# Kernel optimization log

Measured on AMD Instinct MI355X. Metric: run time of the kernel, lower is better.

The kernel has to match this reference:

```python
import jax, jax.numpy as jnp
import numpy as np

B = 262144
L = 12      # seq_len
P = 4       # num_ports
H = 64      # hidden_dim
S = 3       # num_stages
EPS = 1e-8


def setup_inputs() -> dict:
    key = jax.random.key(0)
    ks = jax.random.split(key, 8)
    def w(k, shape, fan_in):
        return jax.random.normal(k, shape, dtype=jnp.float32) / np.sqrt(fan_in)
    return {
        "y_real": jax.random.normal(ks[0], (B, L), dtype=jnp.float32),
        "y_imag": jax.random.normal(ks[1], (B, L), dtype=jnp.float32),
        # weights batched over (stage, port, real/imag branch)
        "W1": w(ks[2], (S, P, 2, 2 * L, H), 2 * L),
        "b1": w(ks[3], (S, P, 2, H), 2 * L),
        "W2": w(ks[4], (S, P, 2, H, H), H),
        "b2": w(ks[5], (S, P, 2, H), H),
        "W3": w(ks[6], (S, P, 2, H, L), H),
        "b3": w(ks[7], (S, P, 2, L), H),
    }


def reference(y_real, y_imag, W1, b1, W2, b2, W3, b3):
    # energy normalization: e = sqrt(mean(|y|^2))
    e = jnp.sqrt(jnp.mean(y_real * y_real + y_imag * y_imag, axis=-1, keepdims=True))  # (B,1)
    yr = y_real / (e + EPS)
    yi = y_imag / (e + EPS)

    n_stages, n_ports = W1.shape[0], W1.shape[1]
    fr = jnp.broadcast_to(yr[:, None, :], (yr.shape[0], n_ports, yr.shape[1]))  # (B,P,L)
    fi = jnp.broadcast_to(yi[:, None, :], (yi.shape[0], n_ports, yi.shape[1]))

    for s in range(n_stages):
        x = jnp.concatenate([fr, fi], axis=-1)                       # (B,P,2L) = cat(real, imag)
        h = jax.nn.relu(jnp.einsum('bpi,pcih->bpch', x, W1[s]) + b1[s])   # (B,P,2,H)
        h = jax.nn.relu(jnp.einsum('bpch,pchg->bpcg', h, W2[s]) + b2[s])  # (B,P,2,H)
        out = jnp.einsum('bpch,pchl->bpcl', h, W3[s]) + b3[s]        # (B,P,2,L)
        fr, fi = out[:, :, 0, :], out[:, :, 1, :]
        # residual coupling: residual = y_norm - sum_p features_p
        rr = yr - fr.sum(axis=1)
        ri = yi - fi.sum(axis=1)
        fr = fr + rr[:, None, :]
        fi = fi + ri[:, None, :]

    fr = fr * e[:, None, :]
    fi = fi * e[:, None, :]
    # complex output represented as trailing real/imag channel: (B,P,L,2)
    return jnp.stack([fr, fi], axis=-1)
```

## Files before the change

kernel.cpp:

```cpp
#include <hip/hip_runtime.h>
#include <hip/hip_bf16.h>

typedef __attribute__((ext_vector_type(8))) short bf16x8;
typedef __attribute__((ext_vector_type(4))) float f32x4;
typedef __attribute__((ext_vector_type(4))) unsigned int u32x4;
typedef unsigned long long ull;

#define RT 64
#define NB (262144 / RT)
#define XSTR 32
#define NFRAG 19

#define X_OFF 0
#define O_OFF 16384
#define Y_OFF 41344
#define E_OFF 47488
#define SMEM_BYTES 47744

__device__ __forceinline__ unsigned pk2(float lo, float hi) {
  union { float f; unsigned u; } a, b;
  a.f = lo; b.f = hi;
  return __builtin_amdgcn_perm(b.u + 0x8000u, a.u + 0x8000u, 0x07060302u);
}
__device__ __forceinline__ unsigned pk2t(float lo, float hi) {
  union { float f; unsigned u; } a, b;
  a.f = lo; b.f = hi;
  return __builtin_amdgcn_perm(b.u, a.u, 0x07060302u);
}
__device__ __forceinline__ bf16x8 mkfrag(unsigned w0, unsigned w1, unsigned w2, unsigned w3) {
  union { bf16x8 v; unsigned u[4]; } U;
  U.u[0] = w0; U.u[1] = w1; U.u[2] = w2; U.u[3] = w3;
  return U.v;
}
__device__ __forceinline__ f32x4 mfma16(bf16x8 a, bf16x8 b, f32x4 c) {
  return __builtin_amdgcn_mfma_f32_16x16x32_bf16(a, b, c, 0, 0, 0);
}

__global__ void wpack(const float* __restrict__ W1, const float* __restrict__ b1,
                      const float* __restrict__ W2, const float* __restrict__ b2,
                      const float* __restrict__ W3, const float* __restrict__ b3,
                      u32x4* __restrict__ ws)
{
  const int pc = blockIdx.x;
  const int lane = threadIdx.x;
  const int q = lane & 15, g = lane >> 4;
  int mpsi[4];
  #pragma unroll
  for (int mt = 0; mt < 4; ++mt)
    mpsi[mt] = 32*(mt>>1) + 8*(q>>2) + 4*(mt&1) + (q&3);

  const float* W1g = W1 + pc * 24 * 64;
  const float* b1g = b1 + pc * 64;
  const float* W2g = W2 + pc * 64 * 64;
  const float* b2g = b2 + pc * 64;
  const float* W3g = W3 + pc * 64 * 12;
  const float* b3g = b3 + pc * 12;
  u32x4* dst = ws + pc * NFRAG * 64 + lane;

  #pragma unroll
  for (int mt = 0; mt < 4; ++mt) {
    unsigned u[4];
    #pragma unroll
    for (int wq = 0; wq < 4; ++wq) {
      int k0 = 8*g + 2*wq;
      float v0 = (k0 < 24) ? W1g[k0*64 + mpsi[mt]] : ((k0 == 24) ? b1g[mpsi[mt]] : 0.f);
      float v1 = (k0+1 < 24) ? W1g[(k0+1)*64 + mpsi[mt]] : 0.f;
      u[wq] = pk2(v0, v1);
    }
    u32x4 t; t[0]=u[0]; t[1]=u[1]; t[2]=u[2]; t[3]=u[3];
    dst[mt * 64] = t;
  }
  #pragma unroll
  for (int kt = 0; kt < 2; ++kt)
    #pragma unroll
    for (int mt = 0; mt < 4; ++mt) {
      unsigned u[4];
      #pragma unroll
      for (int wq = 0; wq < 4; ++wq) {
        int k0 = 32*kt + 8*g + 2*wq;
        u[wq] = pk2(W2g[k0*64 + mpsi[mt]], W2g[(k0+1)*64 + mpsi[mt]]);
      }
      u32x4 t; t[0]=u[0]; t[1]=u[1]; t[2]=u[2]; t[3]=u[3];
      dst[(4 + kt*4 + mt) * 64] = t;
    }
  #pragma unroll
  for (int kt = 0; kt < 2; ++kt) {
    unsigned u[4];
    #pragma unroll
    for (int wq = 0; wq < 4; ++wq) {
      int k0 = 32*kt + 8*g + 2*wq;
      float v0 = (q < 12) ? W3g[k0*12 + q]     : 0.f;
      float v1 = (q < 12) ? W3g[(k0+1)*12 + q] : 0.f;
      u[wq] = pk2(v0, v1);
    }
    u32x4 t; t[0]=u[0]; t[1]=u[1]; t[2]=u[2]; t[3]=u[3];
    dst[(12 + kt) * 64] = t;
  }
  #pragma unroll
  for (int mt = 0; mt < 4; ++mt) {
    f32x4 bv;
    #pragma unroll
    for (int r = 0; r < 4; ++r) bv[r] = b2g[32*(mt>>1) + 8*g + 4*(mt&1) + r];
    union { f32x4 f; u32x4 u; } U; U.f = bv;
    dst[(14 + mt) * 64] = U.u;
  }
  {
    f32x4 bv;
    #pragma unroll
    for (int r = 0; r < 4; ++r) {
      int m = 4*g + r;
      bv[r] = (m < 12) ? b3g[m] : 0.f;
    }
    union { f32x4 f; u32x4 u; } U; U.f = bv;
    dst[18 * 64] = U.u;
  }
}

__global__ __launch_bounds__(256, 3) void rrsep(
    const float* __restrict__ y_real, const float* __restrict__ y_imag,
    const u32x4* __restrict__ wsf, float* __restrict__ out)
{
  __shared__ __align__(16) char smem[SMEM_BYTES];
  unsigned short* xs = (unsigned short*)(smem + X_OFF);
  float*          os = (float*)(smem + O_OFF);
  float*          ysf = (float*)(smem + Y_OFF);
  float*          es = (float*)(smem + E_OFF);

  const int tid  = (int)threadIdx.x;
  const int lane = tid & 63;
  const int p    = tid >> 6;
  const int q    = lane & 15;
  const int g    = lane >> 4;
  const long r0  = (long)blockIdx.x * RT;

  {
    float* stg = (float*)smem;
    if (tid < 192) {
      ((f32x4*)stg)[tid]         = ((const f32x4*)(y_real + r0 * 12))[tid];
      ((f32x4*)(stg + 768))[tid] = ((const f32x4*)(y_imag + r0 * 12))[tid];
    }
    __syncthreads();
    float yv[24]; float ev = 0.f, inv = 0.f;
    if (tid < RT) {
      float acc = 0.f;
      #pragma unroll
      for (int l = 0; l < 12; ++l) {
        yv[l]      = stg[tid * 12 + l];
        yv[12 + l] = stg[768 + tid * 12 + l];
        acc += yv[l] * yv[l] + yv[12 + l] * yv[12 + l];
      }
      ev  = sqrtf(acc * (1.f / 12.f));
      inv = 1.f / (ev + 1e-8f);
    }
    __syncthreads();
    if (tid < RT) {
      es[tid] = ev;
      #pragma unroll
      for (int i = 0; i < 6; ++i) {
        f32x4 t;
        t[0] = yv[4*i+0] * inv; t[1] = yv[4*i+1] * inv;
        t[2] = yv[4*i+2] * inv; t[3] = yv[4*i+3] * inv;
        int l0 = 4*i;
        float* yr = ysf + ((l0 < 12) ? (0 * RT + tid) * 12 + l0 : (1 * RT + tid) * 12 + (l0 - 12));
        *(f32x4*)yr = t;
      }
      unsigned pkw[12];
      #pragma unroll
      for (int j = 0; j < 12; ++j) pkw[j] = pk2(yv[2*j] * inv, yv[2*j+1] * inv);
      #pragma unroll
      for (int p2 = 0; p2 < 4; ++p2) {
        u32x4* xr = (u32x4*)(xs + (p2 * RT + tid) * XSTR);
        u32x4 t0; t0[0]=pkw[0]; t0[1]=pkw[1]; t0[2]=pkw[2]; t0[3]=pkw[3];
        u32x4 t1; t1[0]=pkw[4]; t1[1]=pkw[5]; t1[2]=pkw[6]; t1[3]=pkw[7];
        u32x4 t2; t2[0]=pkw[8]; t2[1]=pkw[9]; t2[2]=pkw[10]; t2[3]=pkw[11];
        u32x4 t3; t3[0]=pk2(1.f, 0.f); t3[1]=0u; t3[2]=0u; t3[3]=0u;
        xr[0]=t0; xr[1]=t1; xr[2]=t2; xr[3]=t3;
      }
    }
    __syncthreads();
  }

  #pragma unroll 1
  for (int s = 0; s < 3; ++s) {
    #pragma unroll 1
    for (int cc = 0; cc < 2; ++cc) {
      const int pc = (s * 4 + p) * 2 + cc;
      const u32x4* wb = wsf + pc * NFRAG * 64 + lane;

      bf16x8 w1f[4], w2f[2][4], w3f[2];
      f32x4 b2f[4], b3f;
      #pragma unroll
      for (int mt = 0; mt < 4; ++mt) {
        union { u32x4 u; bf16x8 v; } U; U.u = wb[mt * 64];
        w1f[mt] = U.v;
      }
      #pragma unroll
      for (int kt = 0; kt < 2; ++kt)
        #pragma unroll
        for (int mt = 0; mt < 4; ++mt) {
          union { u32x4 u; bf16x8 v; } U; U.u = wb[(4 + kt*4 + mt) * 64];
          w2f[kt][mt] = U.v;
        }
      #pragma unroll
      for (int kt = 0; kt < 2; ++kt) {
        union { u32x4 u; bf16x8 v; } U; U.u = wb[(12 + kt) * 64];
        w3f[kt] = U.v;
      }
      #pragma unroll
      for (int mt = 0; mt < 4; ++mt) {
        union { u32x4 u; f32x4 f; } U; U.u = wb[(14 + mt) * 64];
        b2f[mt] = U.f;
      }
      {
        union { u32x4 u; f32x4 f; } U; U.u = wb[18 * 64];
        b3f = U.f;
      }

      #pragma unroll 2
      for (int ch = 0; ch < RT / 16; ++ch) {
        const int row = ch * 16 + q;
        bf16x8 xb = *(const bf16x8*)(xs + (p * RT + row) * XSTR + 8 * g);

        f32x4 c1[4];
        #pragma unroll
        for (int mt = 0; mt < 4; ++mt) c1[mt] = mfma16(w1f[mt], xb, f32x4{0.f,0.f,0.f,0.f});

        bf16x8 fr1[2];
        #pragma unroll
        for (int kt = 0; kt < 2; ++kt)
          fr1[kt] = mkfrag(
            pk2t(fmaxf(c1[2*kt][0], 0.f),   fmaxf(c1[2*kt][1], 0.f)),
            pk2t(fmaxf(c1[2*kt][2], 0.f),   fmaxf(c1[2*kt][3], 0.f)),
            pk2t(fmaxf(c1[2*kt+1][0], 0.f), fmaxf(c1[2*kt+1][1], 0.f)),
            pk2t(fmaxf(c1[2*kt+1][2], 0.f), fmaxf(c1[2*kt+1][3], 0.f)));

        f32x4 c2[4];
        #pragma unroll
        for (int mt = 0; mt < 4; ++mt) {
          c2[mt] = mfma16(w2f[0][mt], fr1[0], b2f[mt]);
          c2[mt] = mfma16(w2f[1][mt], fr1[1], c2[mt]);
        }
        bf16x8 fr2[2];
        #pragma unroll
        for (int kt = 0; kt < 2; ++kt)
          fr2[kt] = mkfrag(
            pk2t(fmaxf(c2[2*kt][0], 0.f),   fmaxf(c2[2*kt][1], 0.f)),
            pk2t(fmaxf(c2[2*kt][2], 0.f),   fmaxf(c2[2*kt][3], 0.f)),
            pk2t(fmaxf(c2[2*kt+1][0], 0.f), fmaxf(c2[2*kt+1][1], 0.f)),
            pk2t(fmaxf(c2[2*kt+1][2], 0.f), fmaxf(c2[2*kt+1][3], 0.f)));

        f32x4 c3 = mfma16(w3f[0], fr2[0], b3f);
        c3 = mfma16(w3f[1], fr2[1], c3);

        if (g < 3)
          *(f32x4*)(os + ((p * 2 + cc) * 65 + row) * 12 + 4 * g) = c3;
      }
    }
    __syncthreads();

    {
      const int r = tid >> 2, pp = tid & 3;
      float sum[24], own[24], yn[24];
      #pragma unroll
      for (int k = 0; k < 24; ++k) sum[k] = 0.f;
      #pragma unroll
      for (int pp2 = 0; pp2 < 4; ++pp2)
        #pragma unroll
        for (int cc2 = 0; cc2 < 2; ++cc2) {
          const f32x4* orow = (const f32x4*)(os + ((pp2 * 2 + cc2) * 65 + r) * 12);
          #pragma unroll
          for (int i = 0; i < 3; ++i) {
            f32x4 t = orow[i];
            sum[cc2*12 + 4*i + 0] += t[0];
            sum[cc2*12 + 4*i + 1] += t[1];
            sum[cc2*12 + 4*i + 2] += t[2];
            sum[cc2*12 + 4*i + 3] += t[3];
          }
        }
      #pragma unroll
      for (int cc2 = 0; cc2 < 2; ++cc2) {
        const f32x4* orow = (const f32x4*)(os + ((pp * 2 + cc2) * 65 + r) * 12);
        const f32x4* yrow = (const f32x4*)(ysf + (cc2 * RT + r) * 12);
        #pragma unroll
        for (int i = 0; i < 3; ++i) {
          f32x4 t = orow[i], u = yrow[i];
          own[cc2*12 + 4*i + 0] = t[0]; yn[cc2*12 + 4*i + 0] = u[0];
          own[cc2*12 + 4*i + 1] = t[1]; yn[cc2*12 + 4*i + 1] = u[1];
          own[cc2*12 + 4*i + 2] = t[2]; yn[cc2*12 + 4*i + 2] = u[2];
          own[cc2*12 + 4*i + 3] = t[3]; yn[cc2*12 + 4*i + 3] = u[3];
        }
      }
      if (s < 2) {
        unsigned xw[12];
        #pragma unroll
        for (int j = 0; j < 12; ++j) {
          float v0 = own[2*j]   + (yn[2*j]   - sum[2*j]);
          float v1 = own[2*j+1] + (yn[2*j+1] - sum[2*j+1]);
          xw[j] = pk2(v0, v1);
        }
        u32x4* xr = (u32x4*)(xs + (pp * RT + r) * XSTR);
        u32x4 t0; t0[0]=xw[0]; t0[1]=xw[1]; t0[2]=xw[2];  t0[3]=xw[3];
        u32x4 t1; t1[0]=xw[4]; t1[1]=xw[5]; t1[2]=xw[6];  t1[3]=xw[7];
        u32x4 t2; t2[0]=xw[8]; t2[1]=xw[9]; t2[2]=xw[10]; t2[3]=xw[11];
        xr[0]=t0; xr[1]=t1; xr[2]=t2;
        __syncthreads();
      } else {
        const float ev = es[r];
        float vals[24];
        #pragma unroll
        for (int l = 0; l < 12; ++l) {
          vals[2*l]   = (own[l]      + yn[l]      - sum[l])      * ev;
          vals[2*l+1] = (own[12 + l] + yn[12 + l] - sum[12 + l]) * ev;
        }
        __syncthreads();
        float* vstg = (float*)smem;
        f32x4* vw = (f32x4*)(vstg + r * 96 + pp * 24);
        #pragma unroll
        for (int i = 0; i < 6; ++i) {
          f32x4 t; t[0]=vals[4*i]; t[1]=vals[4*i+1]; t[2]=vals[4*i+2]; t[3]=vals[4*i+3];
          vw[i] = t;
        }
        __syncthreads();
        const f32x4* vp = (const f32x4*)vstg;
        f32x4* og = (f32x4*)(out + r0 * 96);
        #pragma unroll
        for (int i = 0; i < 6; ++i) og[tid + 256 * i] = vp[tid + 256 * i];
      }
    }
  }
}

extern "C" void kernel_launch(void* const* d_in, const int* in_sizes, int n_in,
                              void* d_out, int out_size, void* d_ws, size_t ws_size,
                              hipStream_t stream) {
  const float* y_real = (const float*)d_in[0];
  const float* y_imag = (const float*)d_in[1];
  const float* W1 = (const float*)d_in[2];
  const float* b1 = (const float*)d_in[3];
  const float* W2 = (const float*)d_in[4];
  const float* b2 = (const float*)d_in[5];
  const float* W3 = (const float*)d_in[6];
  const float* b3 = (const float*)d_in[7];
  float* out = (float*)d_out;
  u32x4* ws = (u32x4*)d_ws;

  hipLaunchKernelGGL(wpack, dim3(24), dim3(64), 0, stream,
                     W1, b1, W2, b2, W3, b3, ws);
  hipLaunchKernelGGL(rrsep, dim3(NB), dim3(256), 0, stream,
                     y_real, y_imag, ws, out);
}
```

Measured before the change: 148.9 us.

## Do residual coupling per real/imag branch to shrink LDS and raise occupancy

Moves the residual reduction inside the per-branch loop so only one branch's MLP outputs sit in shared memory at a time. The real-part result is held in registers until the imaginary part is computed. This cuts the shared-memory footprint, and launch bounds are raised to four blocks per CU. In exchange it adds barriers per stage and tighter register limits, which could cause spills.

After: 156.3 us. 5.0% more time.

```diff
diff --git a/kernel.cpp b/kernel.cpp
--- a/kernel.cpp
+++ b/kernel.cpp
@@ -12,10 +12,10 @@
 #define NFRAG 19
 
 #define X_OFF 0
-#define O_OFF 16384
-#define Y_OFF 41344
-#define E_OFF 47488
-#define SMEM_BYTES 47744
+#define OC_OFF 16384
+#define Y_OFF 28864
+#define E_OFF 35008
+#define SMEM_BYTES 35264
 
 __device__ __forceinline__ unsigned pk2(float lo, float hi) {
   union { float f; unsigned u; } a, b;
@@ -116,13 +116,13 @@
   }
 }
 
-__global__ __launch_bounds__(256, 3) void rrsep(
+__global__ __launch_bounds__(256, 4) void rrsep(
     const float* __restrict__ y_real, const float* __restrict__ y_imag,
     const u32x4* __restrict__ wsf, float* __restrict__ out)
 {
   __shared__ __align__(16) char smem[SMEM_BYTES];
   unsigned short* xs = (unsigned short*)(smem + X_OFF);
-  float*          os = (float*)(smem + O_OFF);
+  float*          oc = (float*)(smem + OC_OFF);
   float*          ysf = (float*)(smem + Y_OFF);
   float*          es = (float*)(smem + E_OFF);
 
@@ -182,6 +182,9 @@
 
   #pragma unroll 1
   for (int s = 0; s < 3; ++s) {
+    unsigned xr0[6];
+    float valsR[12];
+
     #pragma unroll 1
     for (int cc = 0; cc < 2; ++cc) {
       const int pc = (s * 4 + p) * 2 + cc;
@@ -253,78 +256,82 @@
         c3 = mfma16(w3f[1], fr2[1], c3);
 
         if (g < 3)
-          *(f32x4*)(os + ((p * 2 + cc) * 65 + row) * 12 + 4 * g) = c3;
-      }
-    }
-    __syncthreads();
-
-    {
-      const int r = tid >> 2, pp = tid & 3;
-      float sum[24], own[24], yn[24];
-      #pragma unroll
-      for (int k = 0; k < 24; ++k) sum[k] = 0.f;
-      #pragma unroll
-      for (int pp2 = 0; pp2 < 4; ++pp2)
-        #pragma unroll
-        for (int cc2 = 0; cc2 < 2; ++cc2) {
-          const f32x4* orow = (const f32x4*)(os + ((pp2 * 2 + cc2) * 65 + r) * 12);
+          *(f32x4*)(oc + (p * 65 + row) * 12 + 4 * g) = c3;
+      }
+      __syncthreads();
+
+      {
+        const int r = tid >> 2, pp = tid & 3;
+        float sum[12], own[12], yn[12];
+        #pragma unroll
+        for (int k = 0; k < 12; ++k) sum[k] = 0.f;
+        #pragma unroll
+        for (int pp2 = 0; pp2 < 4; ++pp2) {
+          const f32x4* orow = (const f32x4*)(oc + (pp2 * 65 + r) * 12);
           #pragma unroll
           for (int i = 0; i < 3; ++i) {
             f32x4 t = orow[i];
-            sum[cc2*12 + 4*i + 0] += t[0];
-            sum[cc2*12 + 4*i + 1] += t[1];
-            sum[cc2*12 + 4*i + 2] += t[2];
-            sum[cc2*12 + 4*i + 3] += t[3];
-          }
-        }
-      #pragma unroll
-      for (int cc2 = 0; cc2 < 2; ++cc2) {
-        const f32x4* orow = (const f32x4*)(os + ((pp * 2 + cc2) * 65 + r) * 12);
-        const f32x4* yrow = (const f32x4*)(ysf + (cc2 * RT + r) * 12);
-        #pragma unroll
-        for (int i = 0; i < 3; ++i) {
-          f32x4 t = orow[i], u = yrow[i];
-          own[cc2*12 + 4*i + 0] = t[0]; yn[cc2*12 + 4*i + 0] = u[0];
-          own[cc2*12 + 4*i + 1] = t[1]; yn[cc2*12 + 4*i + 1] = u[1];
-          own[cc2*12 + 4*i + 2] = t[2]; yn[cc2*12 + 4*i + 2] = u[2];
-          own[cc2*12 + 4*i + 3] = t[3]; yn[cc2*12 + 4*i + 3] = u[3];
-        }
-      }
-      if (s < 2) {
-        unsigned xw[12];
-        #pragma unroll
-        for (int j = 0; j < 12; ++j) {
-          float v0 = own[2*j]   + (yn[2*j]   - sum[2*j]);
-          float v1 = own[2*j+1] + (yn[2*j+1] - sum[2*j+1]);
-          xw[j] = pk2(v0, v1);
-        }
-        u32x4* xr = (u32x4*)(xs + (pp * RT + r) * XSTR);
-        u32x4 t0; t0[0]=xw[0]; t0[1]=xw[1]; t0[2]=xw[2];  t0[3]=xw[3];
-        u32x4 t1; t1[0]=xw[4]; t1[1]=xw[5]; t1[2]=xw[6];  t1[3]=xw[7];
-        u32x4 t2; t2[0]=xw[8]; t2[1]=xw[9]; t2[2]=xw[10]; t2[3]=xw[11];
-        xr[0]=t0; xr[1]=t1; xr[2]=t2;
-        __syncthreads();
-      } else {
-        const float ev = es[r];
-        float vals[24];
-        #pragma unroll
-        for (int l = 0; l < 12; ++l) {
-          vals[2*l]   = (own[l]      + yn[l]      - sum[l])      * ev;
-          vals[2*l+1] = (own[12 + l] + yn[12 + l] - sum[12 + l]) * ev;
-        }
-        __syncthreads();
-        float* vstg = (float*)smem;
-        f32x4* vw = (f32x4*)(vstg + r * 96 + pp * 24);
-        #pragma unroll
-        for (int i = 0; i < 6; ++i) {
-          f32x4 t; t[0]=vals[4*i]; t[1]=vals[4*i+1]; t[2]=vals[4*i+2]; t[3]=vals[4*i+3];
-          vw[i] = t;
-        }
-        __syncthreads();
-        const f32x4* vp = (const f32x4*)vstg;
-        f32x4* og = (f32x4*)(out + r0 * 96);
-        #pragma unroll
-        for (int i = 0; i < 6; ++i) og[tid + 256 * i] = vp[tid + 256 * i];
+            sum[4*i+0] += t[0]; sum[4*i+1] += t[1];
+            sum[4*i+2] += t[2]; sum[4*i+3] += t[3];
+          }
+        }
+        {
+          const f32x4* orow = (const f32x4*)(oc + (pp * 65 + r) * 12);
+          const f32x4* yrow = (const f32x4*)(ysf + (cc * RT + r) * 12);
+          #pragma unroll
+          for (int i = 0; i < 3; ++i) {
+            f32x4 t = orow[i], u = yrow[i];
+            own[4*i+0] = t[0]; yn[4*i+0] = u[0];
+            own[4*i+1] = t[1]; yn[4*i+1] = u[1];
+            own[4*i+2] = t[2]; yn[4*i+2] = u[2];
+            own[4*i+3] = t[3]; yn[4*i+3] = u[3];
+          }
+        }
+        if (s < 2) {
+          float xh[12];
+          #pragma unroll
+          for (int j = 0; j < 12; ++j) xh[j] = own[j] + (yn[j] - sum[j]);
+          if (cc == 0) {
+            #pragma unroll
+            for (int i = 0; i < 6; ++i) xr0[i] = pk2(xh[2*i], xh[2*i+1]);
+          } else {
+            unsigned xi[6];
+            #pragma unroll
+            for (int i = 0; i < 6; ++i) xi[i] = pk2(xh[2*i], xh[2*i+1]);
+            u32x4* xr = (u32x4*)(xs + (pp * RT + r) * XSTR);
+            u32x4 t0; t0[0]=xr0[0]; t0[1]=xr0[1]; t0[2]=xr0[2]; t0[3]=xr0[3];
+            u32x4 t1; t1[0]=xr0[4]; t1[1]=xr0[5]; t1[2]=xi[0];  t1[3]=xi[1];
+            u32x4 t2; t2[0]=xi[2];  t2[1]=xi[3];  t2[2]=xi[4];  t2[3]=xi[5];
+            xr[0]=t0; xr[1]=t1; xr[2]=t2;
+          }
+          __syncthreads();
+        } else if (cc == 0) {
+          const float ev = es[r];
+          #pragma unroll
+          for (int l = 0; l < 12; ++l) valsR[l] = (own[l] + yn[l] - sum[l]) * ev;
+          __syncthreads();
+        } else {
+          const float ev = es[r];
+          float vals[24];
+          #pragma unroll
+          for (int l = 0; l < 12; ++l) {
+            vals[2*l]   = valsR[l];
+            vals[2*l+1] = (own[l] + yn[l] - sum[l]) * ev;
+          }
+          __syncthreads();
+          float* vstg = (float*)smem;
+          f32x4* vw = (f32x4*)(vstg + r * 96 + pp * 24);
+          #pragma unroll
+          for (int i = 0; i < 6; ++i) {
+            f32x4 t; t[0]=vals[4*i]; t[1]=vals[4*i+1]; t[2]=vals[4*i+2]; t[3]=vals[4*i+3];
+            vw[i] = t;
+          }
+          __syncthreads();
+          const f32x4* vp = (const f32x4*)vstg;
+          f32x4* og = (f32x4*)(out + r0 * 96);
+          #pragma unroll
+          for (int i = 0; i < 6; ++i) og[tid + 256 * i] = vp[tid + 256 * i];
+        }
       }
     }
   }
```

## Make each wave own rows across all ports, removing block barriers and LDS reduction

Applied to the files above, without the earlier changes.

Reassigns work so each wave processes 32 rows through all four ports and both branches, instead of one port per wave over 64 shared rows. The cross-port residual sum is then done in registers from the MFMA outputs, which removes the per-stage shared-memory output buffer and all __syncthreads. Input normalization becomes per-wave with shuffles, normalized y is kept as bf16 in LDS, and outputs are written straight to global without a staging buffer. In exchange each wave reloads weights for all 8 port/branch combos per stage, keeps more registers live, and loses the coalesced staged global stores.

After: 184.8 us. +24.2%, slower.

```diff
diff --git a/kernel.cpp b/kernel.cpp
--- a/kernel.cpp
+++ b/kernel.cpp
@@ -6,16 +6,15 @@
 typedef __attribute__((ext_vector_type(4))) unsigned int u32x4;
 typedef unsigned long long ull;
 
-#define RT 64
+#define RT 128
 #define NB (262144 / RT)
-#define XSTR 32
 #define NFRAG 19
 
-#define X_OFF 0
-#define O_OFF 16384
-#define Y_OFF 41344
-#define E_OFF 47488
-#define SMEM_BYTES 47744
+#define WREG 12032
+#define SMEM_BYTES (4 * WREG)
+#define XW_OFF 0
+#define YW_OFF 10240
+#define EW_OFF 11776
 
 __device__ __forceinline__ unsigned pk2(float lo, float hi) {
   union { float f; unsigned u; } a, b;
@@ -26,6 +25,14 @@
   union { float f; unsigned u; } a, b;
   a.f = lo; b.f = hi;
   return __builtin_amdgcn_perm(b.u, a.u, 0x07060302u);
+}
+__device__ __forceinline__ void unp4(ull v, float* d) {
+  unsigned a = (unsigned)v, b = (unsigned)(v >> 32);
+  union { unsigned u; float f; } x;
+  x.u = a << 16;         d[0] = x.f;
+  x.u = a & 0xffff0000u; d[1] = x.f;
+  x.u = b << 16;         d[2] = x.f;
+  x.u = b & 0xffff0000u; d[3] = x.f;
 }
 __device__ __forceinline__ bf16x8 mkfrag(unsigned w0, unsigned w1, unsigned w2, unsigned w3) {
   union { bf16x8 v; unsigned u[4]; } U;
@@ -121,210 +128,192 @@
     const u32x4* __restrict__ wsf, float* __restrict__ out)
 {
   __shared__ __align__(16) char smem[SMEM_BYTES];
-  unsigned short* xs = (unsigned short*)(smem + X_OFF);
-  float*          os = (float*)(smem + O_OFF);
-  float*          ysf = (float*)(smem + Y_OFF);
-  float*          es = (float*)(smem + E_OFF);
-
   const int tid  = (int)threadIdx.x;
   const int lane = tid & 63;
-  const int p    = tid >> 6;
+  const int w    = tid >> 6;
   const int q    = lane & 15;
   const int g    = lane >> 4;
-  const long r0  = (long)blockIdx.x * RT;
+  char* wbase = smem + w * WREG;
+  unsigned short* xw = (unsigned short*)(wbase + XW_OFF);
+  char*           yw = wbase + YW_OFF;
+  float*          ew = (float*)(wbase + EW_OFF);
+  const long wr0 = (long)blockIdx.x * RT + w * 32;
 
   {
-    float* stg = (float*)smem;
-    if (tid < 192) {
-      ((f32x4*)stg)[tid]         = ((const f32x4*)(y_real + r0 * 12))[tid];
-      ((f32x4*)(stg + 768))[tid] = ((const f32x4*)(y_imag + r0 * 12))[tid];
-    }
-    __syncthreads();
-    float yv[24]; float ev = 0.f, inv = 0.f;
-    if (tid < RT) {
-      float acc = 0.f;
-      #pragma unroll
-      for (int l = 0; l < 12; ++l) {
-        yv[l]      = stg[tid * 12 + l];
-        yv[12 + l] = stg[768 + tid * 12 + l];
-        acc += yv[l] * yv[l] + yv[12 + l] * yv[12 + l];
-      }
-      ev  = sqrtf(acc * (1.f / 12.f));
-      inv = 1.f / (ev + 1e-8f);
-    }
-    __syncthreads();
-    if (tid < RT) {
-      es[tid] = ev;
-      #pragma unroll
-      for (int i = 0; i < 6; ++i) {
-        f32x4 t;
-        t[0] = yv[4*i+0] * inv; t[1] = yv[4*i+1] * inv;
-        t[2] = yv[4*i+2] * inv; t[3] = yv[4*i+3] * inv;
-        int l0 = 4*i;
-        float* yr = ysf + ((l0 < 12) ? (0 * RT + tid) * 12 + l0 : (1 * RT + tid) * 12 + (l0 - 12));
-        *(f32x4*)yr = t;
-      }
-      unsigned pkw[12];
-      #pragma unroll
-      for (int j = 0; j < 12; ++j) pkw[j] = pk2(yv[2*j] * inv, yv[2*j+1] * inv);
-      #pragma unroll
-      for (int p2 = 0; p2 < 4; ++p2) {
-        u32x4* xr = (u32x4*)(xs + (p2 * RT + tid) * XSTR);
-        u32x4 t0; t0[0]=pkw[0]; t0[1]=pkw[1]; t0[2]=pkw[2]; t0[3]=pkw[3];
-        u32x4 t1; t1[0]=pkw[4]; t1[1]=pkw[5]; t1[2]=pkw[6]; t1[3]=pkw[7];
-        u32x4 t2; t2[0]=pkw[8]; t2[1]=pkw[9]; t2[2]=pkw[10]; t2[3]=pkw[11];
-        u32x4 t3; t3[0]=pk2(1.f, 0.f); t3[1]=0u; t3[2]=0u; t3[3]=0u;
-        xr[0]=t0; xr[1]=t1; xr[2]=t2; xr[3]=t3;
-      }
-    }
-    __syncthreads();
+    #pragma unroll
+    for (int ch = 0; ch < 2; ++ch) {
+      const int row = 16 * ch + q;
+      f32x4 v0 = {0.f,0.f,0.f,0.f}, v1 = {0.f,0.f,0.f,0.f};
+      if (g < 3) {
+        v0 = *(const f32x4*)(y_real + (wr0 + row) * 12 + 4 * g);
+        v1 = *(const f32x4*)(y_imag + (wr0 + row) * 12 + 4 * g);
+      }
+      float acc = v0[0]*v0[0]+v0[1]*v0[1]+v0[2]*v0[2]+v0[3]*v0[3]
+                + v1[0]*v1[0]+v1[1]*v1[1]+v1[2]*v1[2]+v1[3]*v1[3];
+      acc += __shfl_xor(acc, 16);
+      acc += __shfl_xor(acc, 32);
+      const float e   = sqrtf(acc * (1.f / 12.f));
+      const float inv = 1.f / (e + 1e-8f);
+      if (g == 0) ew[row] = e;
+      if (g < 3) {
+        unsigned a0 = pk2(v0[0]*inv, v0[1]*inv), a1 = pk2(v0[2]*inv, v0[3]*inv);
+        unsigned b0 = pk2(v1[0]*inv, v1[1]*inv), b1 = pk2(v1[2]*inv, v1[3]*inv);
+        *(ull*)(yw + row * 24 + 8 * g)       = (ull)a0 | ((ull)a1 << 32);
+        *(ull*)(yw + 768 + row * 24 + 8 * g) = (ull)b0 | ((ull)b1 << 32);
+        #pragma unroll
+        for (int p = 0; p < 4; ++p) {
+          char* xrp = (char*)xw + p * 2560 + row * 80;
+          *(ull*)(xrp + 8 * g)      = (ull)a0 | ((ull)a1 << 32);
+          *(ull*)(xrp + 24 + 8 * g) = (ull)b0 | ((ull)b1 << 32);
+        }
+      } else {
+        u32x4 t; t[0] = pk2(1.f, 0.f); t[1] = 0u; t[2] = 0u; t[3] = 0u;
+        #pragma unroll
+        for (int p = 0; p < 4; ++p)
+          *(u32x4*)((char*)xw + p * 2560 + row * 80 + 48) = t;
+      }
+    }
   }
 
   #pragma unroll 1
   for (int s = 0; s < 3; ++s) {
-    #pragma unroll 1
-    for (int cc = 0; cc < 2; ++cc) {
-      const int pc = (s * 4 + p) * 2 + cc;
-      const u32x4* wb = wsf + pc * NFRAG * 64 + lane;
-
-      bf16x8 w1f[4], w2f[2][4], w3f[2];
-      f32x4 b2f[4], b3f;
+    unsigned stash[4][2][2];
+    f32x4 vc0[4][2];
+
+    #pragma unroll
+    for (int c = 0; c < 2; ++c) {
+      f32x4 o[4][2];
+
       #pragma unroll
-      for (int mt = 0; mt < 4; ++mt) {
-        union { u32x4 u; bf16x8 v; } U; U.u = wb[mt * 64];
-        w1f[mt] = U.v;
-      }
+      for (int p = 0; p < 4; ++p) {
+        const u32x4* wb = wsf + ((s * 4 + p) * 2 + c) * NFRAG * 64 + lane;
+        bf16x8 w1f[4], w2f[2][4], w3f[2];
+        f32x4 b2f[4], b3f;
+        #pragma unroll
+        for (int mt = 0; mt < 4; ++mt) {
+          union { u32x4 u; bf16x8 v; } U; U.u = wb[mt * 64];
+          w1f[mt] = U.v;
+        }
+        #pragma unroll
+        for (int kt = 0; kt < 2; ++kt)
+          #pragma unroll
+          for (int mt = 0; mt < 4; ++mt) {
+            union { u32x4 u; bf16x8 v; } U; U.u = wb[(4 + kt*4 + mt) * 64];
+            w2f[kt][mt] = U.v;
+          }
+        #pragma unroll
+        for (int kt = 0; kt < 2; ++kt) {
+          union { u32x4 u; bf16x8 v; } U; U.u = wb[(12 + kt) * 64];
+          w3f[kt] = U.v;
+        }
+        #pragma unroll
+        for (int mt = 0; mt < 4; ++mt) {
+          union { u32x4 u; f32x4 f; } U; U.u = wb[(14 + mt) * 64];
+          b2f[mt] = U.f;
+        }
+        {
+          union { u32x4 u; f32x4 f; } U; U.u = wb[18 * 64];
+          b3f = U.f;
+        }
+
+        #pragma unroll
+        for (int ch = 0; ch < 2; ++ch) {
+          const int row = 16 * ch + q;
+          bf16x8 xb = *(const bf16x8*)((char*)xw + p * 2560 + row * 80 + 16 * g);
+
+          f32x4 c1[4];
+          #pragma unroll
+          for (int mt = 0; mt < 4; ++mt) c1[mt] = mfma16(w1f[mt], xb, f32x4{0.f,0.f,0.f,0.f});
+
+          bf16x8 fr1[2];
+          #pragma unroll
+          for (int kt = 0; kt < 2; ++kt)
+            fr1[kt] = mkfrag(
+              pk2t(fmaxf(c1[2*kt][0], 0.f),   fmaxf(c1[2*kt][1], 0.f)),
+              pk2t(fmaxf(c1[2*kt][2], 0.f),   fmaxf(c1[2*kt][3], 0.f)),
+              pk2t(fmaxf(c1[2*kt+1][0], 0.f), fmaxf(c1[2*kt+1][1], 0.f)),
+              pk2t(fmaxf(c1[2*kt+1][2], 0.f), fmaxf(c1[2*kt+1][3], 0.f)));
+
+          f32x4 c2[4];
+          #pragma unroll
+          for (int mt = 0; mt < 4; ++mt) {
+            c2[mt] = mfma16(w2f[0][mt], fr1[0], b2f[mt]);
+            c2[mt] = mfma16(w2f[1][mt], fr1[1], c2[mt]);
+          }
+          bf16x8 fr2[2];
+          #pragma unroll
+          for (int kt = 0; kt < 2; ++kt)
+            fr2[kt] = mkfrag(
+              pk2t(fmaxf(c2[2*kt][0], 0.f),   fmaxf(c2[2*kt][1], 0.f)),
+              pk2t(fmaxf(c2[2*kt][2], 0.f),   fmaxf(c2[2*kt][3], 0.f)),
+              pk2t(fmaxf(c2[2*kt+1][0], 0.f), fmaxf(c2[2*kt+1][1], 0.f)),
+              pk2t(fmaxf(c2[2*kt+1][2], 0.f), fmaxf(c2[2*kt+1][3], 0.f)));
+
+          f32x4 c3 = mfma16(w3f[0], fr2[0], b3f);
+          c3 = mfma16(w3f[1], fr2[1], c3);
+          o[p][ch] = c3;
+        }
+      }
+
       #pragma unroll
-      for (int kt = 0; kt < 2; ++kt)
-        #pragma unroll
-        for (int mt = 0; mt < 4; ++mt) {
-          union { u32x4 u; bf16x8 v; } U; U.u = wb[(4 + kt*4 + mt) * 64];
-          w2f[kt][mt] = U.v;
-        }
-      #pragma unroll
-      for (int kt = 0; kt < 2; ++kt) {
-        union { u32x4 u; bf16x8 v; } U; U.u = wb[(12 + kt) * 64];
-        w3f[kt] = U.v;
-      }
-      #pragma unroll
-      for (int mt = 0; mt < 4; ++mt) {
-        union { u32x4 u; f32x4 f; } U; U.u = wb[(14 + mt) * 64];
-        b2f[mt] = U.f;
-      }
-      {
-        union { u32x4 u; f32x4 f; } U; U.u = wb[18 * 64];
-        b3f = U.f;
-      }
-
-      #pragma unroll 2
-      for (int ch = 0; ch < RT / 16; ++ch) {
-        const int row = ch * 16 + q;
-        bf16x8 xb = *(const bf16x8*)(xs + (p * RT + row) * XSTR + 8 * g);
-
-        f32x4 c1[4];
-        #pragma unroll
-        for (int mt = 0; mt < 4; ++mt) c1[mt] = mfma16(w1f[mt], xb, f32x4{0.f,0.f,0.f,0.f});
-
-        bf16x8 fr1[2];
-        #pragma unroll
-        for (int kt = 0; kt < 2; ++kt)
-          fr1[kt] = mkfrag(
-            pk2t(fmaxf(c1[2*kt][0], 0.f),   fmaxf(c1[2*kt][1], 0.f)),
-            pk2t(fmaxf(c1[2*kt][2], 0.f),   fmaxf(c1[2*kt][3], 0.f)),
-            pk2t(fmaxf(c1[2*kt+1][0], 0.f), fmaxf(c1[2*kt+1][1], 0.f)),
-            pk2t(fmaxf(c1[2*kt+1][2], 0.f), fmaxf(c1[2*kt+1][3], 0.f)));
-
-        f32x4 c2[4];
-        #pragma unroll
-        for (int mt = 0; mt < 4; ++mt) {
-          c2[mt] = mfma16(w2f[0][mt], fr1[0], b2f[mt]);
-          c2[mt] = mfma16(w2f[1][mt], fr1[1], c2[mt]);
-        }
-        bf16x8 fr2[2];
-        #pragma unroll
-        for (int kt = 0; kt < 2; ++kt)
-          fr2[kt] = mkfrag(
-            pk2t(fmaxf(c2[2*kt][0], 0.f),   fmaxf(c2[2*kt][1], 0.f)),
-            pk2t(fmaxf(c2[2*kt][2], 0.f),   fmaxf(c2[2*kt][3], 0.f)),
-            pk2t(fmaxf(c2[2*kt+1][0], 0.f), fmaxf(c2[2*kt+1][1], 0.f)),
-            pk2t(fmaxf(c2[2*kt+1][2], 0.f), fmaxf(c2[2*kt+1][3], 0.f)));
-
-        f32x4 c3 = mfma16(w3f[0], fr2[0], b3f);
-        c3 = mfma16(w3f[1], fr2[1], c3);
-
-        if (g < 3)
-          *(f32x4*)(os + ((p * 2 + cc) * 65 + row) * 12 + 4 * g) = c3;
-      }
-    }
-    __syncthreads();
-
-    {
-      const int r = tid >> 2, pp = tid & 3;
-      float sum[24], own[24], yn[24];
-      #pragma unroll
-      for (int k = 0; k < 24; ++k) sum[k] = 0.f;
-      #pragma unroll
-      for (int pp2 = 0; pp2 < 4; ++pp2)
-        #pragma unroll
-        for (int cc2 = 0; cc2 < 2; ++cc2) {
-          const f32x4* orow = (const f32x4*)(os + ((pp2 * 2 + cc2) * 65 + r) * 12);
-          #pragma unroll
-          for (int i = 0; i < 3; ++i) {
-            f32x4 t = orow[i];
-            sum[cc2*12 + 4*i + 0] += t[0];
-            sum[cc2*12 + 4*i + 1] += t[1];
-            sum[cc2*12 + 4*i + 2] += t[2];
-            sum[cc2*12 + 4*i + 3] += t[3];
+      for (int ch = 0; ch < 2; ++ch) {
+        const int row = 16 * ch + q;
+        f32x4 sum;
+        #pragma unroll
+        for (int j = 0; j < 4; ++j)
+          sum[j] = o[0][ch][j] + o[1][ch][j] + o[2][ch][j] + o[3][ch][j];
+        if (g < 3) {
+          float yn[4];
+          unp4(*(const ull*)(yw + c * 768 + row * 24 + 8 * g), yn);
+          f32x4 rr;
+          #pragma unroll
+          for (int j = 0; j < 4; ++j) rr[j] = yn[j] - sum[j];
+
+          if (s < 2) {
+            if (c == 0) {
+              #pragma unroll
+              for (int p = 0; p < 4; ++p) {
+                f32x4 nx;
+                #pragma unroll
+                for (int j = 0; j < 4; ++j) nx[j] = o[p][ch][j] + rr[j];
+                stash[p][ch][0] = pk2(nx[0], nx[1]);
+                stash[p][ch][1] = pk2(nx[2], nx[3]);
+              }
+            } else {
+              #pragma unroll
+              for (int p = 0; p < 4; ++p) {
+                f32x4 nx;
+                #pragma unroll
+                for (int j = 0; j < 4; ++j) nx[j] = o[p][ch][j] + rr[j];
+                char* xrp = (char*)xw + p * 2560 + row * 80;
+                *(ull*)(xrp + 8 * g) = (ull)stash[p][ch][0] | ((ull)stash[p][ch][1] << 32);
+                unsigned i0 = pk2(nx[0], nx[1]), i1 = pk2(nx[2], nx[3]);
+                *(ull*)(xrp + 24 + 8 * g) = (ull)i0 | ((ull)i1 << 32);
+              }
+            }
+          } else {
+            const float e = ew[row];
+            if (c == 0) {
+              #pragma unroll
+              for (int p = 0; p < 4; ++p) {
+                #pragma unroll
+                for (int j = 0; j < 4; ++j) vc0[p][ch][j] = (o[p][ch][j] + rr[j]) * e;
+              }
+            } else {
+              float* ob = out + (wr0 + row) * 96 + 8 * g;
+              #pragma unroll
+              for (int p = 0; p < 4; ++p) {
+                f32x4 A, B;
+                A[0] = vc0[p][ch][0]; A[1] = (o[p][ch][0] + rr[0]) * e;
+                A[2] = vc0[p][ch][1]; A[3] = (o[p][ch][1] + rr[1]) * e;
+                B[0] = vc0[p][ch][2]; B[1] = (o[p][ch][2] + rr[2]) * e;
+                B[2] = vc0[p][ch][3]; B[3] = (o[p][ch][3] + rr[3]) * e;
+                *(f32x4*)(ob + p * 24)     = A;
+                *(f32x4*)(ob + p * 24 + 4) = B;
+              }
+            }
           }
         }
-      #pragma unroll
-      for (int cc2 = 0; cc2 < 2; ++cc2) {
-        const f32x4* orow = (const f32x4*)(os + ((pp * 2 + cc2) * 65 + r) * 12);
-        const f32x4* yrow = (const f32x4*)(ysf + (cc2 * RT + r) * 12);
-        #pragma unroll
-        for (int i = 0; i < 3; ++i) {
-          f32x4 t = orow[i], u = yrow[i];
-          own[cc2*12 + 4*i + 0] = t[0]; yn[cc2*12 + 4*i + 0] = u[0];
-          own[cc2*12 + 4*i + 1] = t[1]; yn[cc2*12 + 4*i + 1] = u[1];
-          own[cc2*12 + 4*i + 2] = t[2]; yn[cc2*12 + 4*i + 2] = u[2];
-          own[cc2*12 + 4*i + 3] = t[3]; yn[cc2*12 + 4*i + 3] = u[3];
-        }
-      }
-      if (s < 2) {
-        unsigned xw[12];
-        #pragma unroll
-        for (int j = 0; j < 12; ++j) {
-          float v0 = own[2*j]   + (yn[2*j]   - sum[2*j]);
-          float v1 = own[2*j+1] + (yn[2*j+1] - sum[2*j+1]);
-          xw[j] = pk2(v0, v1);
-        }
-        u32x4* xr = (u32x4*)(xs + (pp * RT + r) * XSTR);
-        u32x4 t0; t0[0]=xw[0]; t0[1]=xw[1]; t0[2]=xw[2];  t0[3]=xw[3];
-        u32x4 t1; t1[0]=xw[4]; t1[1]=xw[5]; t1[2]=xw[6];  t1[3]=xw[7];
-        u32x4 t2; t2[0]=xw[8]; t2[1]=xw[9]; t2[2]=xw[10]; t2[3]=xw[11];
-        xr[0]=t0; xr[1]=t1; xr[2]=t2;
-        __syncthreads();
-      } else {
-        const float ev = es[r];
-        float vals[24];
-        #pragma unroll
-        for (int l = 0; l < 12; ++l) {
-          vals[2*l]   = (own[l]      + yn[l]      - sum[l])      * ev;
-          vals[2*l+1] = (own[12 + l] + yn[12 + l] - sum[12 + l]) * ev;
-        }
-        __syncthreads();
-        float* vstg = (float*)smem;
-        f32x4* vw = (f32x4*)(vstg + r * 96 + pp * 24);
-        #pragma unroll
-        for (int i = 0; i < 6; ++i) {
-          f32x4 t; t[0]=vals[4*i]; t[1]=vals[4*i+1]; t[2]=vals[4*i+2]; t[3]=vals[4*i+3];
-          vw[i] = t;
-        }
-        __syncthreads();
-        const f32x4* vp = (const f32x4*)vstg;
-        f32x4* og = (f32x4*)(out + r0 * 96);
-        #pragma unroll
-        for (int i = 0; i < 6; ++i) og[tid + 256 * i] = vp[tid + 256 * i];
       }
     }
   }
```
